# Kernel optimization log

Measured on AMD Instinct MI355X. Metric: run time of the kernel, lower is better.

The kernel has to match this reference:

```python
import jax, jax.numpy as jnp
import numpy as np


def _next_pow2(n: int) -> int:
    return int(2 ** int(np.ceil(np.log2(n))))


def setup_inputs() -> dict:
    key = jax.random.key(0)
    kx, kk = jax.random.split(key)
    B, SEQ_LEN, N_FILTERS, KLEN = 128, 8192, 20, 769
    x = jax.random.normal(kx, (B, 1, SEQ_LEN), dtype=jnp.float32)
    # filter bank buffer (FIR kernels, one per (pha|amp) band), stands in for
    # design_filter_tensorpac output padded to common max length
    kernels = jax.random.normal(kk, (N_FILTERS, KLEN), dtype=jnp.float32) * 0.05
    return {"x": x, "kernels": kernels}


def reference(x, kernels):
    # OptimizedBandPassFilter.forward with use_fft=True, edge_mode=None
    B, _, seq_len = x.shape
    n_filters, klen = kernels.shape
    fft_size = _next_pow2(seq_len + klen - 1)  # 16384

    # _prepare_fft_filters: zero-pad kernels to fft_size, rfft
    kernels_fft = jnp.fft.rfft(kernels, n=fft_size, axis=-1)  # [F, fft/2+1]

    # _fft_filter: squeeze channel dim, zero-pad signal, rfft
    x2 = x[:, 0, :]  # [B, S]
    x_fft = jnp.fft.rfft(x2, n=fft_size, axis=-1)  # [B, fft/2+1]

    # broadcast complex multiply across filter bank, inverse rfft, crop
    filtered_fft = x_fft[:, None, :] * kernels_fft[None, :, :]  # [B, F, fft/2+1]
    filtered = jnp.fft.irfft(filtered_fft, n=fft_size, axis=-1)[..., :seq_len]

    # final unsqueeze(1) -> [B, 1, F, S]
    return filtered[:, None, :, :]
```

## Files before the change

kernel.cpp:

```cpp
#include <hip/hip_runtime.h>
#include <hip/hip_bf16.h>


#define BATCH 128
#define SEQ   8192
#define NF    20
#define KLEN  769

#define THREADS 512
#define CHUNK   2048
#define NCHUNK  (SEQ / CHUNK)
#define KT      25

#define HSTRIDE_B 1616
#define XSTRIDE_B 5776
#define XN        2864
#define XBYTES    (8 * XSTRIDE_B)
#define HBYTES    (32 * HSTRIDE_B)
#define LDSB      (XBYTES + HBYTES)

typedef short bf16x8 __attribute__((ext_vector_type(8)));
typedef float f32x16 __attribute__((ext_vector_type(16)));

static __device__ __forceinline__ unsigned short f2bf(float v) {
    __hip_bfloat16 h = __float2bfloat16(v);
    return *reinterpret_cast<unsigned short*>(&h);
}

__global__ __launch_bounds__(THREADS, 2)
void bpf_mfma(const float* __restrict__ xg, const float* __restrict__ kg,
              float* __restrict__ out) {
    extern __shared__ char smem[];
    char* xs = smem;
    char* hs = smem + XBYTES;

    const int tid = threadIdx.x;
    const int bid = blockIdx.x;
    const int b   = bid >> 2;
    const int T0  = (bid & 3) * CHUNK;
    const int E0  = T0 - 800;

    for (int idx = tid; idx < 32 * 800; idx += THREADS) {
        int f = idx / 800;
        int p = idx - f * 800;
        int k = 791 - p;
        float v = 0.0f;
        if (f < NF && k >= 0 && k < KLEN) v = kg[f * KLEN + k];
        *reinterpret_cast<unsigned short*>(hs + f * HSTRIDE_B + 2 * p) = f2bf(v);
    }
    const float* xb = xg + (size_t)b * SEQ;
    for (int rho = 0; rho < 8; ++rho) {
        char* xr = xs + rho * XSTRIDE_B;
        for (int e = tid; e < XN; e += THREADS) {
            int g = E0 + rho + e;
            float v = (g >= 0 && g < SEQ) ? xb[g] : 0.0f;
            *reinterpret_cast<unsigned short*>(xr + 2 * e) = f2bf(v);
        }
    }
    __syncthreads();

    const int lane = tid & 63;
    const int wid  = tid >> 6;
    const int c    = lane & 31;
    const int g2   = lane >> 5;

    const char* Abase = hs + c * HSTRIDE_B - 16 * g2;

    float* outb = out + (size_t)b * NF * SEQ;

    for (int ti = 0; ti < 2; ++ti) {
        const int n0     = T0 + (wid + 8 * ti) * 128;
        const int s_base = n0 + c + 1 - 8 * g2 - 784;
        const int rho    = s_base & 7;
        const int ebase  = s_base - rho - E0;
        const char* Bbase = xs + rho * XSTRIDE_B + 2 * ebase;

        f32x16 acc[4];
#pragma unroll
        for (int wt = 0; wt < 4; ++wt)
#pragma unroll
            for (int r = 0; r < 16; ++r) acc[wt][r] = 0.0f;

        bf16x8 ring[4][2];
#pragma unroll
        for (int wt = 0; wt < 4; ++wt) {
            ring[(4 - wt) & 3][0] = *reinterpret_cast<const bf16x8*>(Bbase + 1568 + 64 * wt);
            ring[(4 - wt) & 3][1] = *reinterpret_cast<const bf16x8*>(Bbase + 1536 + 64 * wt);
        }

#pragma unroll
        for (int i = 0; i < KT; ++i) {
            bf16x8 na, nb;
            if (i < KT - 1) {
                na = *reinterpret_cast<const bf16x8*>(Bbase + 64 * (23 - i) + 32);
                nb = *reinterpret_cast<const bf16x8*>(Bbase + 64 * (23 - i));
            }
            bf16x8 a0 = *reinterpret_cast<const bf16x8*>(Abase + 1584 - 64 * i);
            bf16x8 a1 = *reinterpret_cast<const bf16x8*>(Abase + 1552 - 64 * i);
#pragma unroll
            for (int wt = 0; wt < 4; ++wt) {
                acc[wt] = __builtin_amdgcn_mfma_f32_32x32x16_bf16(
                    a0, ring[(i - wt) & 3][0], acc[wt], 0, 0, 0);
                acc[wt] = __builtin_amdgcn_mfma_f32_32x32x16_bf16(
                    a1, ring[(i - wt) & 3][1], acc[wt], 0, 0, 0);
            }
            if (i < KT - 1) {
                ring[(i + 1) & 3][0] = na;
                ring[(i + 1) & 3][1] = nb;
            }
        }

#pragma unroll
        for (int wt = 0; wt < 4; ++wt) {
            const int tcol = n0 + 32 * wt + c;
#pragma unroll
            for (int r = 0; r < 16; ++r) {
                const int f = (r & 3) + 8 * (r >> 2) + 4 * g2;
                if (f < NF) outb[f * SEQ + tcol] = acc[wt][r];
            }
        }
    }
}

extern "C" void kernel_launch(void* const* d_in, const int* in_sizes, int n_in,
                              void* d_out, int out_size, void* d_ws, size_t ws_size,
                              hipStream_t stream) {
    const float* x    = (const float*)d_in[0];
    const float* kern = (const float*)d_in[1];
    float* out = (float*)d_out;

    (void)d_ws; (void)ws_size; (void)in_sizes; (void)n_in; (void)out_size;

    hipFuncSetAttribute(reinterpret_cast<const void*>(bpf_mfma),
                        hipFuncAttributeMaxDynamicSharedMemorySize, LDSB);
    bpf_mfma<<<BATCH * NCHUNK, THREADS, LDSB, stream>>>(x, kern, out);
}
```

Baseline: 155.2 us.

## Precompute bf16 filter and shifted signal copies in workspace, use larger blocks

Two new prep kernels convert the filter bank and the 8 phase-shifted copies of each signal row to bf16 in workspace, once per call. The main kernel then fills LDS with vectorized 16-byte copies instead of scalar per-element conversion with integer division, and the redundant per-block filter conversion is removed. Blocks grow to 1024 threads covering 4096 outputs each, so 256 blocks replace 512. The MFMA loop is reordered to issue all a0 products before the a1 products. The old kernel stays as a fallback when the workspace is too small, and the new path costs two extra launches plus a workspace round trip.

After: 215.2 us. +38.6%, slower.

```diff
diff --git a/kernel.cpp b/kernel.cpp
--- a/kernel.cpp
+++ b/kernel.cpp
@@ -7,18 +7,6 @@
 #define NF    20
 #define KLEN  769
 
-#define THREADS 512
-#define CHUNK   2048
-#define NCHUNK  (SEQ / CHUNK)
-#define KT      25
-
-#define HSTRIDE_B 1616
-#define XSTRIDE_B 5776
-#define XN        2864
-#define XBYTES    (8 * XSTRIDE_B)
-#define HBYTES    (32 * HSTRIDE_B)
-#define LDSB      (XBYTES + HBYTES)
-
 typedef short bf16x8 __attribute__((ext_vector_type(8)));
 typedef float f32x16 __attribute__((ext_vector_type(16)));
 
@@ -27,20 +15,154 @@
     return *reinterpret_cast<unsigned short*>(&h);
 }
 
-__global__ __launch_bounds__(THREADS, 2)
-void bpf_mfma(const float* __restrict__ xg, const float* __restrict__ kg,
-              float* __restrict__ out) {
+#define HSTRIDE_B 1616
+#define XROW_B    18016
+#define XBSTRIDE_B 144128
+#define WS_X_OFF  65536
+#define WS_REQ    (WS_X_OFF + (size_t)BATCH * XBSTRIDE_B)
+
+__global__ void bpf_prep_h(const float* __restrict__ kg, char* __restrict__ hdst) {
+    const int f = blockIdx.x;
+    for (int p = threadIdx.x; p < 808; p += blockDim.x) {
+        int k = 791 - p;
+        float v = (f < NF && k >= 0 && k < KLEN) ? kg[f * KLEN + k] : 0.0f;
+        *reinterpret_cast<unsigned short*>(hdst + f * HSTRIDE_B + 2 * p) = f2bf(v);
+    }
+}
+
+__global__ void bpf_prep_x(const float* __restrict__ xg, char* __restrict__ xdst) {
+    const int y   = blockIdx.y;
+    const int b   = y >> 3;
+    const int rho = y & 7;
+    const int q0  = (blockIdx.x * blockDim.x + threadIdx.x) * 8;
+    if (q0 >= 9008) return;
+    const float* xb = xg + (size_t)b * SEQ;
+    const int base = q0 - 800 + rho;
+    bf16x8 v;
+#pragma unroll
+    for (int j = 0; j < 8; ++j) {
+        int g = base + j;
+        float f = (g >= 0 && g < SEQ) ? xb[g] : 0.0f;
+        v[j] = (short)f2bf(f);
+    }
+    *reinterpret_cast<bf16x8*>(xdst + (size_t)y * XROW_B + 2 * q0) = v;
+}
+
+#define V2_THREADS 1024
+#define XS_LDS   9872
+#define XREGION  (8 * XS_LDS)
+#define V2_LDSB  (XREGION + 32 * HSTRIDE_B)
+#define KT       25
+
+__global__ __launch_bounds__(V2_THREADS, 4)
+void bpf_mfma_v2(const char* __restrict__ xsrc_all, const char* __restrict__ hsrc,
+                 float* __restrict__ out) {
     extern __shared__ char smem[];
     char* xs = smem;
-    char* hs = smem + XBYTES;
+    char* hs = smem + XREGION;
 
     const int tid = threadIdx.x;
-    const int bid = blockIdx.x;
-    const int b   = bid >> 2;
-    const int T0  = (bid & 3) * CHUNK;
+    const int b   = blockIdx.x >> 1;
+    const int T0  = (blockIdx.x & 1) * 4096;
+
+    for (int v = tid; v < 3232; v += V2_THREADS) {
+        *reinterpret_cast<bf16x8*>(hs + v * 16) =
+            *reinterpret_cast<const bf16x8*>(hsrc + v * 16);
+    }
+    {
+        const char* xsrcb = xsrc_all + (size_t)b * XBSTRIDE_B + 2 * T0;
+        if (tid < 614) {
+#pragma unroll
+            for (int rho = 0; rho < 8; ++rho) {
+                *reinterpret_cast<bf16x8*>(xs + rho * XS_LDS + tid * 16) =
+                    *reinterpret_cast<const bf16x8*>(xsrcb + rho * XROW_B + tid * 16);
+            }
+        }
+    }
+    __syncthreads();
+
+    const int lane = tid & 63;
+    const int wid  = tid >> 6;
+    const int c    = lane & 31;
+    const int g2   = lane >> 5;
+
+    const char* Abase = hs + c * HSTRIDE_B - 16 * g2;
+    float* outb = out + (size_t)b * NF * SEQ;
+
+    for (int ti = 0; ti < 2; ++ti) {
+        const int n0     = T0 + (wid + 16 * ti) * 128;
+        const int s_base = n0 + c + 1 - 8 * g2 - 784;
+        const int rho    = s_base & 7;
+        const int ebase  = s_base - rho - (T0 - 800);
+        const char* Bbase = xs + rho * XS_LDS + 2 * ebase;
+
+        f32x16 acc[4];
+#pragma unroll
+        for (int wt = 0; wt < 4; ++wt)
+#pragma unroll
+            for (int r = 0; r < 16; ++r) acc[wt][r] = 0.0f;
+
+        bf16x8 ring[4][2];
+#pragma unroll
+        for (int wt = 0; wt < 4; ++wt) {
+            ring[(4 - wt) & 3][0] = *reinterpret_cast<const bf16x8*>(Bbase + 1568 + 64 * wt);
+            ring[(4 - wt) & 3][1] = *reinterpret_cast<const bf16x8*>(Bbase + 1536 + 64 * wt);
+        }
+
+#pragma unroll
+        for (int i = 0; i < KT; ++i) {
+            bf16x8 na, nb;
+            if (i < KT - 1) {
+                na = *reinterpret_cast<const bf16x8*>(Bbase + 64 * (23 - i) + 32);
+                nb = *reinterpret_cast<const bf16x8*>(Bbase + 64 * (23 - i));
+            }
+            bf16x8 a0 = *reinterpret_cast<const bf16x8*>(Abase + 1584 - 64 * i);
+            bf16x8 a1 = *reinterpret_cast<const bf16x8*>(Abase + 1552 - 64 * i);
+#pragma unroll
+            for (int wt = 0; wt < 4; ++wt)
+                acc[wt] = __builtin_amdgcn_mfma_f32_32x32x16_bf16(
+                    a0, ring[(i - wt) & 3][0], acc[wt], 0, 0, 0);
+#pragma unroll
+            for (int wt = 0; wt < 4; ++wt)
+                acc[wt] = __builtin_amdgcn_mfma_f32_32x32x16_bf16(
+                    a1, ring[(i - wt) & 3][1], acc[wt], 0, 0, 0);
+            if (i < KT - 1) {
+                ring[(i + 1) & 3][0] = na;
+                ring[(i + 1) & 3][1] = nb;
+            }
+        }
+
+#pragma unroll
+        for (int wt = 0; wt < 4; ++wt) {
+            const int tcol = n0 + 32 * wt + c;
+#pragma unroll
+            for (int r = 0; r < 16; ++r) {
+                const int f = (r & 3) + 8 * (r >> 2) + 4 * g2;
+                if (f < NF) outb[f * SEQ + tcol] = acc[wt][r];
+            }
+        }
+    }
+}
+
+#define FB_THREADS 512
+#define FB_XSTRIDE 5776
+#define FB_XN      2864
+#define FB_XBYTES  (8 * FB_XSTRIDE)
+#define FB_LDSB    (FB_XBYTES + 32 * HSTRIDE_B)
+
+__global__ __launch_bounds__(FB_THREADS, 2)
+void bpf_mfma_fb(const float* __restrict__ xg, const float* __restrict__ kg,
+                 float* __restrict__ out) {
+    extern __shared__ char smem[];
+    char* xs = smem;
+    char* hs = smem + FB_XBYTES;
+
+    const int tid = threadIdx.x;
+    const int b   = blockIdx.x >> 2;
+    const int T0  = (blockIdx.x & 3) * 2048;
     const int E0  = T0 - 800;
 
-    for (int idx = tid; idx < 32 * 800; idx += THREADS) {
+    for (int idx = tid; idx < 32 * 800; idx += FB_THREADS) {
         int f = idx / 800;
         int p = idx - f * 800;
         int k = 791 - p;
@@ -50,8 +172,8 @@
     }
     const float* xb = xg + (size_t)b * SEQ;
     for (int rho = 0; rho < 8; ++rho) {
-        char* xr = xs + rho * XSTRIDE_B;
-        for (int e = tid; e < XN; e += THREADS) {
+        char* xr = xs + rho * FB_XSTRIDE;
+        for (int e = tid; e < FB_XN; e += FB_THREADS) {
             int g = E0 + rho + e;
             float v = (g >= 0 && g < SEQ) ? xb[g] : 0.0f;
             *reinterpret_cast<unsigned short*>(xr + 2 * e) = f2bf(v);
@@ -63,9 +185,7 @@
     const int wid  = tid >> 6;
     const int c    = lane & 31;
     const int g2   = lane >> 5;
-
     const char* Abase = hs + c * HSTRIDE_B - 16 * g2;
-
     float* outb = out + (size_t)b * NF * SEQ;
 
     for (int ti = 0; ti < 2; ++ti) {
@@ -73,7 +193,7 @@
         const int s_base = n0 + c + 1 - 8 * g2 - 784;
         const int rho    = s_base & 7;
         const int ebase  = s_base - rho - E0;
-        const char* Bbase = xs + rho * XSTRIDE_B + 2 * ebase;
+        const char* Bbase = xs + rho * FB_XSTRIDE + 2 * ebase;
 
         f32x16 acc[4];
 #pragma unroll
@@ -87,7 +207,6 @@
             ring[(4 - wt) & 3][0] = *reinterpret_cast<const bf16x8*>(Bbase + 1568 + 64 * wt);
             ring[(4 - wt) & 3][1] = *reinterpret_cast<const bf16x8*>(Bbase + 1536 + 64 * wt);
         }
-
 #pragma unroll
         for (int i = 0; i < KT; ++i) {
             bf16x8 na, nb;
@@ -98,18 +217,18 @@
             bf16x8 a0 = *reinterpret_cast<const bf16x8*>(Abase + 1584 - 64 * i);
             bf16x8 a1 = *reinterpret_cast<const bf16x8*>(Abase + 1552 - 64 * i);
 #pragma unroll
-            for (int wt = 0; wt < 4; ++wt) {
+            for (int wt = 0; wt < 4; ++wt)
                 acc[wt] = __builtin_amdgcn_mfma_f32_32x32x16_bf16(
                     a0, ring[(i - wt) & 3][0], acc[wt], 0, 0, 0);
+#pragma unroll
+            for (int wt = 0; wt < 4; ++wt)
                 acc[wt] = __builtin_amdgcn_mfma_f32_32x32x16_bf16(
                     a1, ring[(i - wt) & 3][1], acc[wt], 0, 0, 0);
-            }
             if (i < KT - 1) {
                 ring[(i + 1) & 3][0] = na;
                 ring[(i + 1) & 3][1] = nb;
             }
         }
-
 #pragma unroll
         for (int wt = 0; wt < 4; ++wt) {
             const int tcol = n0 + 32 * wt + c;
@@ -128,10 +247,18 @@
     const float* x    = (const float*)d_in[0];
     const float* kern = (const float*)d_in[1];
     float* out = (float*)d_out;
-
-    (void)d_ws; (void)ws_size; (void)in_sizes; (void)n_in; (void)out_size;
-
-    hipFuncSetAttribute(reinterpret_cast<const void*>(bpf_mfma),
-                        hipFuncAttributeMaxDynamicSharedMemorySize, LDSB);
-    bpf_mfma<<<BATCH * NCHUNK, THREADS, LDSB, stream>>>(x, kern, out);
-}
+    (void)in_sizes; (void)n_in; (void)out_size;
+
+    if (ws_size >= WS_REQ) {
+        char* ws = (char*)d_ws;
+        bpf_prep_h<<<32, 256, 0, stream>>>(kern, ws);
+        bpf_prep_x<<<dim3(5, BATCH * 8), 256, 0, stream>>>(x, ws + WS_X_OFF);
+        hipFuncSetAttribute(reinterpret_cast<const void*>(bpf_mfma_v2),
+                            hipFuncAttributeMaxDynamicSharedMemorySize, V2_LDSB);
+        bpf_mfma_v2<<<BATCH * 2, V2_THREADS, V2_LDSB, stream>>>(ws + WS_X_OFF, ws, out);
+    } else {
+        hipFuncSetAttribute(reinterpret_cast<const void*>(bpf_mfma_fb),
+                            hipFuncAttributeMaxDynamicSharedMemorySize, FB_LDSB);
+        bpf_mfma_fb<<<BATCH * 4, FB_THREADS, FB_LDSB, stream>>>(x, kern, out);
+    }
+}
```
